# Kernel optimization log

Measured on AMD Instinct MI355X. Metric: run time of the kernel, lower is better.

The kernel has to match this reference:

```python
import jax, jax.numpy as jnp
import numpy as np

K = 5  # kernel_size


def _unfold(x, k):
    """Torch F.unfold equivalent: [B,C,H,W] -> [B,C,k*k,H,W].
    Patch index is row-major over the kxk window (dy*k+dx), matching
    F.unfold's channel-major / window-row-major layout after view(B,C,k*k,H,W)."""
    p = k // 2
    B, C, H, W = x.shape
    xp = jnp.pad(x, ((0, 0), (0, 0), (p, p), (p, p)))
    patches = [xp[:, :, dy:dy + H, dx:dx + W] for dy in range(k) for dx in range(k)]
    return jnp.stack(patches, axis=2)


def _conv2d(x, w, b, pad):
    y = jax.lax.conv_general_dilated(
        x, w, window_strides=(1, 1), padding=[(pad, pad), (pad, pad)],
        dimension_numbers=("NCHW", "OIHW", "NCHW"))
    return y + b[None, :, None, None]


def setup_inputs() -> dict:
    key = jax.random.key(0)
    k0, k1, k2 = jax.random.split(key, 3)
    B, H, W = 2, 1024, 1024
    flow = jax.random.normal(k0, (B, 2, H, W), jnp.float32)
    # kernel_gen params: Conv2d(3,32,3,pad=1) -> ReLU -> Conv2d(32,50,1)
    w1 = jax.random.normal(k1, (32, 3, 3, 3), jnp.float32) * 0.1
    b1 = jnp.zeros((32,), jnp.float32)
    w2 = jax.random.normal(k2, (K * K * 2, 32, 1, 1), jnp.float32) * 0.1
    b2 = jnp.zeros((K * K * 2,), jnp.float32)
    return {"flow": flow, "w1": w1, "b1": b1, "w2": w2, "b2": b2}


def reference(flow, w1, b1, w2, b2):
    B, _, H, W = flow.shape
    patches = _unfold(flow, K)                       # [B,2,25,H,W]
    # torch .var(dim=2) defaults to unbiased (ddof=1)
    var = jnp.var(patches, axis=2, ddof=1)           # [B,2,H,W]
    consistency = jnp.exp(-jnp.sqrt(jnp.sum(var * var, axis=1, keepdims=True)))  # [B,1,H,W]
    guidance = jnp.concatenate([flow, consistency], axis=1)  # [B,3,H,W]
    h = jax.nn.relu(_conv2d(guidance, w1, b1, pad=1))        # [B,32,H,W]
    kernels = _conv2d(h, w2, b2, pad=0).reshape(B, 2, K * K, H, W)
    refined = jnp.sum(kernels * patches, axis=2)             # [B,2,H,W]
    return refined
```

## Files before the change

### kernel.cpp

```cpp
#include <hip/hip_runtime.h>
#include <math.h>

#define KSZ 5
#define TSX 16
#define TSY 64
#define HALO 3
#define FWX 22
#define FH  70
#define SCH 66
#define PITCH 23
#define SF_C (FH*PITCH)
#define SC_BASE (2*SF_C)
#define SMF_TOT (SC_BASE + SCH*PITCH)

typedef __attribute__((ext_vector_type(8))) short short8_t;
typedef __attribute__((ext_vector_type(4))) float float4_t;
typedef __attribute__((ext_vector_type(2))) unsigned int uint2_t;

static __device__ __forceinline__ unsigned short f2bf(float f) {
    union { float f; unsigned int u; } v; v.f = f;
    return (unsigned short)((v.u + 0x7FFFu + ((v.u >> 16) & 1u)) >> 16);
}
static __device__ __forceinline__ unsigned int pk2t(float a, float b) {
    union { float f; unsigned int u; } ua, ub; ua.f = a; ub.f = b;
    return __builtin_amdgcn_perm(ub.u, ua.u, 0x07060302u);
}
static __device__ __forceinline__ float bflo(unsigned int u) {
    union { unsigned int u; float f; } v; v.u = u << 16; return v.f;
}
static __device__ __forceinline__ float bfhi(unsigned int u) {
    union { unsigned int u; float f; } v; v.u = u & 0xffff0000u; return v.f;
}

static __device__ __forceinline__ void slot_decode(int n, int& c, int& sel, int& idx, bool& valid) {
    int g4c = (n >> 2) & 3;
    c = g4c >> 1; sel = g4c & 1;
    idx = ((n >> 4) << 2) + (n & 3);
    valid = sel ? (idx < 10) : (idx < 15);
}

static __device__ __forceinline__ int kperm(int s) {
    int sg = s >> 3, sj = s & 7;
    if (sg < 3) return sg*9 + sj;
    if (sj == 1) return 8;
    if (sj == 2) return 17;
    if (sj == 4) return 26;
    return -1;
}

static __device__ __forceinline__ int kperm2(int s) {
    int g = s >> 3, j = s & 7;
    return (j < 4) ? (g*4 + j) : (16 + g*4 + (j - 4));
}

__global__ __launch_bounds__(256)
void pack_kernel(const float* __restrict__ w1, const float* __restrict__ b1,
                 const float* __restrict__ w2, const float* __restrict__ b2,
                 unsigned short* __restrict__ wp, float* __restrict__ bp)
{
    const int tid = threadIdx.x;
    for (int i = tid; i < 6*64*8; i += 256) {
        int f = i >> 9, l = (i >> 3) & 63, j = i & 7;
        int m = l & 15, s = ((l >> 4) << 3) + j;
        float v;
        if (f < 2) {
            int k = kperm(s);
            v = (k >= 0) ? w1[(f*16 + m)*27 + k] : 0.f;
        } else {
            int n = (f - 2)*16 + m;
            int c, sel, idx; bool valid;
            slot_decode(n, c, sel, idx, valid);
            v = valid ? w2[(c*25 + sel*15 + idx)*32 + kperm2(s)] : 0.f;
        }
        wp[i] = f2bf(v);
    }
    for (int i = tid; i < 6*64*4; i += 256) {
        int f = i >> 8, l = (i >> 2) & 63, r = i & 3, g4 = l >> 4;
        float v;
        if (f < 2) v = b1[f*16 + g4*4 + r];
        else {
            int n = (f - 2)*16 + g4*4 + r;
            int c, sel, idx; bool valid;
            slot_decode(n, c, sel, idx, valid);
            v = valid ? b2[c*25 + sel*15 + idx] : 0.f;
        }
        bp[i] = v;
    }
}

__global__ __launch_bounds__(256, 5)
void refine_kernel(const float* __restrict__ flow,
                   const unsigned short* __restrict__ wp,
                   const float* __restrict__ bp,
                   float* __restrict__ out, int H, int W)
{
    __shared__ float smf[SMF_TOT];
    __shared__ __align__(8) uint2_t rs[FH*18];

    const int tid = threadIdx.x;
    const int x0 = blockIdx.x * TSX;
    const int y0 = blockIdx.y * TSY;
    const int b  = blockIdx.z;

    const int lane = tid & 63;
    const int wave = tid >> 6;
    const int col  = lane & 15;
    const int g4   = lane >> 4;

    short8_t w1A[2], w2A[4];
    float4_t cb1[2], cb2[4];
    #pragma unroll
    for (int nt = 0; nt < 2; ++nt) {
        w1A[nt] = *(const short8_t*)&wp[(nt*64 + lane)*8];
        cb1[nt] = *(const float4_t*)&bp[(nt*64 + lane)*4];
    }
    #pragma unroll
    for (int nt = 0; nt < 4; ++nt) {
        w2A[nt] = *(const short8_t*)&wp[((2+nt)*64 + lane)*8];
        cb2[nt] = *(const float4_t*)&bp[((2+nt)*64 + lane)*4];
    }

    {
        const float* srcb = flow + (size_t)(b*2) * H * W;
        if (x0 >= 4 && x0 + TSX + 4 <= W && y0 >= HALO && y0 + TSY + HALO <= H) {
            const float* s = srcb + (size_t)(y0 - HALO) * W + (x0 - 4);
            for (int i = tid; i < 2*FH*12; i += 256) {
                int c = 0, r = i;
                if (r >= FH*12) { c = 1; r -= FH*12; }
                int ly = r / 12, lx2 = r - ly*12;
                float2 v = *(const float2*)(s + (size_t)c*H*W + (size_t)ly*W + 2*lx2);
                int dst = c*SF_C + ly*PITCH + 2*lx2 - 1;
                if (dst >= 0) smf[dst] = v.x;
                smf[dst + 1] = v.y;
            }
        } else {
            for (int i = tid; i < 2*FH*FWX; i += 256) {
                int c = 0, r = i;
                if (r >= FH*FWX) { c = 1; r -= FH*FWX; }
                int ly = r / FWX, lx = r - ly*FWX;
                int gy = y0 - HALO + ly, gx = x0 - HALO + lx;
                float v = 0.f;
                if (gy >= 0 && gy < H && gx >= 0 && gx < W)
                    v = srcb[(size_t)c*H*W + (size_t)gy*W + gx];
                smf[c*SF_C + ly*PITCH + lx] = v;
            }
        }
    }
    __syncthreads();

    for (int i = tid; i < FH*9; i += 256) {
        int y = i / 9, xp = (i - y*9) * 2;
        const float* r0 = &smf[y*PITCH + xp];
        const float* r1 = &smf[SF_C + y*PITCH + xp];
        float a0=r0[0], a1=r0[1], a2=r0[2], a3=r0[3], a4=r0[4], a5=r0[5];
        float c0=r1[0], c1=r1[1], c2=r1[2], c3=r1[3], c4=r1[4], c5=r1[5];
        float sA = ((a0+a1)+(a2+a3))+a4;
        float qA = fmaf(a4,a4, fmaf(a3,a3, fmaf(a2,a2, fmaf(a1,a1, a0*a0))));
        float sB = ((c0+c1)+(c2+c3))+c4;
        float qB = fmaf(c4,c4, fmaf(c3,c3, fmaf(c2,c2, fmaf(c1,c1, c0*c0))));
        float sA1 = sA + a5 - a0;
        float qA1 = fmaf(-a0, a0, fmaf(a5, a5, qA));
        float sB1 = sB + c5 - c0;
        float qB1 = fmaf(-c0, c0, fmaf(c5, c5, qB));
        rs[y*18 + xp]     = (uint2_t){pk2t(sA,  qA ), pk2t(sB,  qB )};
        rs[y*18 + xp + 1] = (uint2_t){pk2t(sA1, qA1), pk2t(sB1, qB1)};
    }
    __syncthreads();

    for (int i = tid; i < (SCH/2)*18; i += 256) {
        int u = i / 18, px = i - u*18;
        int py0 = u*2;
        int gx = x0 - 1 + px;
        int gy0 = y0 - 1 + py0;
        const uint2_t* rp = rs + py0*18 + px;
        float4_t f[6];
        #pragma unroll
        for (int k = 0; k < 6; ++k) {
            uint2_t uu = rp[k*18];
            f[k] = (float4_t){bflo(uu.x), bfhi(uu.x), bflo(uu.y), bfhi(uu.y)};
        }
        float4_t mid  = (f[1] + f[2]) + (f[3] + f[4]);
        float4_t acc0 = mid + f[0];
        float4_t acc1 = mid + f[5];
        float cons0 = 0.f, cons1 = 0.f;
        bool okx = (gx >= 0) && (gx < W);
        if (okx && gy0 >= 0 && gy0 < H) {
            float v0 = (acc0.y - acc0.x*acc0.x*(1.f/25.f)) * (1.f/24.f);
            float v1 = (acc0.w - acc0.z*acc0.z*(1.f/25.f)) * (1.f/24.f);
            cons0 = __expf(-sqrtf(v0*v0 + v1*v1));
        }
        if (okx && gy0+1 >= 0 && gy0+1 < H) {
            float v0 = (acc1.y - acc1.x*acc1.x*(1.f/25.f)) * (1.f/24.f);
            float v1 = (acc1.w - acc1.z*acc1.z*(1.f/25.f)) * (1.f/24.f);
            cons1 = __expf(-sqrtf(v0*v0 + v1*v1));
        }
        smf[SC_BASE + py0*PITCH + px]       = cons0;
        smf[SC_BASE + (py0+1)*PITCH + px]   = cons1;
    }
    __syncthreads();

    const int sel = g4 & 1, pc = g4 >> 1;
    const int ty0 = wave*16;

    int gb0, gb1, gb2, gb3;
    {
        int p0 = 0*SF_C + 2*PITCH + (col + 2);
        int p1 = 1*SF_C + 2*PITCH + (col + 2);
        int p2 = SC_BASE + col;
        if (g4 == 0)      { gb0 = gb1 = gb2 = gb3 = p0; }
        else if (g4 == 1) { gb0 = gb1 = gb2 = gb3 = p1; }
        else if (g4 == 2) { gb0 = gb1 = gb2 = gb3 = p2; }
        else { gb0 = p0 + 47; gb1 = p1 + 46; gb2 = p2 + 24; gb3 = p0; }
        gb0 += ty0*PITCH; gb1 += ty0*PITCH; gb2 += ty0*PITCH; gb3 += ty0*PITCH;
    }

    int pb = pc*SF_C + sel*(3*PITCH) + PITCH + 1 + col + ty0*PITCH;
    float pv[15];
    #pragma unroll
    for (int i = 0; i < 15; ++i) pv[i] = smf[pb + (i/5)*PITCH + (i%5)];

    #pragma unroll
    for (int mt = 0; mt < 16; ++mt) {
        float ga = smf[gb0 + 0],  gb_ = smf[gb0 + 1];
        float gc = smf[gb1 + 2],  gd  = smf[gb1 + 23];
        float ge = smf[gb2 + 24], gf  = smf[gb2 + 25];
        float gg = smf[gb3 + 46], gh  = smf[gb3 + 47];
        union { unsigned int u[4]; short8_t s; } gu;
        gu.u[0] = pk2t(ga, gb_); gu.u[1] = pk2t(gc, gd);
        gu.u[2] = pk2t(ge, gf);  gu.u[3] = pk2t(gg, gh);
        gb0 += PITCH; gb1 += PITCH; gb2 += PITCH; gb3 += PITCH;

        float4_t h0 = __builtin_amdgcn_mfma_f32_16x16x32_bf16(w1A[0], gu.s, cb1[0], 0, 0, 0);
        float4_t h1 = __builtin_amdgcn_mfma_f32_16x16x32_bf16(w1A[1], gu.s, cb1[1], 0, 0, 0);

        union { unsigned int u[4]; short8_t s; } hu;
        hu.u[0] = pk2t(fmaxf(h0[0],0.f), fmaxf(h0[1],0.f));
        hu.u[1] = pk2t(fmaxf(h0[2],0.f), fmaxf(h0[3],0.f));
        hu.u[2] = pk2t(fmaxf(h1[0],0.f), fmaxf(h1[1],0.f));
        hu.u[3] = pk2t(fmaxf(h1[2],0.f), fmaxf(h1[3],0.f));

        float4_t ka[4];
        #pragma unroll
        for (int nt = 0; nt < 4; ++nt)
            ka[nt] = __builtin_amdgcn_mfma_f32_16x16x32_bf16(w2A[nt], hu.s, cb2[nt], 0, 0, 0);

        float s = 0.f;
        #pragma unroll
        for (int i = 0; i < 15; ++i)
            s = fmaf(ka[i >> 2][i & 3], pv[i], s);

        if (mt < 15) {
            #pragma unroll
            for (int i = 0; i < 10; ++i) pv[i] = pv[i + 5];
            pb += PITCH;
            #pragma unroll
            for (int i = 10; i < 15; ++i) pv[i] = smf[pb + (i/5)*PITCH + (i%5)];
        }

        s += __shfl_xor(s, 16);

        if (sel == 0) {
            int y = y0 + ty0 + mt, x = x0 + col;
            out[((size_t)(b*2 + pc) * H + y) * W + x] = s;
        }
    }
}

extern "C" void kernel_launch(void* const* d_in, const int* in_sizes, int n_in,
                              void* d_out, int out_size, void* d_ws, size_t ws_size,
                              hipStream_t stream) {
    const float* flow = (const float*)d_in[0];
    const float* w1   = (const float*)d_in[1];
    const float* b1   = (const float*)d_in[2];
    const float* w2   = (const float*)d_in[3];
    const float* b2   = (const float*)d_in[4];
    float* out = (float*)d_out;

    unsigned short* wp = (unsigned short*)d_ws;
    float* bp = (float*)((char*)d_ws + 8192);

    const int H = 1024, W = 1024;
    const int B = in_sizes[0] / (2 * H * W);

    pack_kernel<<<1, 256, 0, stream>>>(w1, b1, w2, b2, wp, bp);
    dim3 grid(W / TSX, H / TSY, B);
    refine_kernel<<<grid, dim3(256), 0, stream>>>(flow, wp, bp, out, H, W);
}
```

Baseline: 109.8 us.

## Split row-sum stage into two halves to shrink LDS and raise occupancy

The horizontal row-sum buffer is cut from 70 rows to 38 by computing the consistency map in two passes, each filling the buffer and then reducing it vertically. The smaller LDS footprint lets the launch bound ask for 6 blocks per CU instead of 5, aiming at better latency hiding. ReLU is also applied as a vector max before packing. The price is two extra barriers and some recomputed halo rows, and the tighter register budget may cause spills.

```diff
diff --git a/kernel.cpp b/kernel.cpp
--- a/kernel.cpp
+++ b/kernel.cpp
@@ -12,6 +12,7 @@
 #define SF_C (FH*PITCH)
 #define SC_BASE (2*SF_C)
 #define SMF_TOT (SC_BASE + SCH*PITCH)
+#define RSROWS 38
 
 typedef __attribute__((ext_vector_type(8))) short short8_t;
 typedef __attribute__((ext_vector_type(4))) float float4_t;
@@ -30,6 +31,13 @@
 }
 static __device__ __forceinline__ float bfhi(unsigned int u) {
     union { unsigned int u; float f; } v; v.u = u & 0xffff0000u; return v.f;
+}
+static __device__ __forceinline__ float4_t relu4(float4_t x) {
+#if __has_builtin(__builtin_elementwise_max)
+    return __builtin_elementwise_max(x, (float4_t){0.f, 0.f, 0.f, 0.f});
+#else
+    return (float4_t){fmaxf(x[0],0.f), fmaxf(x[1],0.f), fmaxf(x[2],0.f), fmaxf(x[3],0.f)};
+#endif
 }
 
 static __device__ __forceinline__ void slot_decode(int n, int& c, int& sel, int& idx, bool& valid) {
@@ -88,14 +96,67 @@
     }
 }
 
-__global__ __launch_bounds__(256, 5)
+static __device__ __forceinline__ void hsum_row(const float* __restrict__ smf,
+                                                uint2_t* __restrict__ rs,
+                                                int y, int slot, int xp)
+{
+    const float* r0 = &smf[y*PITCH + xp];
+    const float* r1 = &smf[SF_C + y*PITCH + xp];
+    float a0=r0[0], a1=r0[1], a2=r0[2], a3=r0[3], a4=r0[4], a5=r0[5];
+    float c0=r1[0], c1=r1[1], c2=r1[2], c3=r1[3], c4=r1[4], c5=r1[5];
+    float sA = ((a0+a1)+(a2+a3))+a4;
+    float qA = fmaf(a4,a4, fmaf(a3,a3, fmaf(a2,a2, fmaf(a1,a1, a0*a0))));
+    float sB = ((c0+c1)+(c2+c3))+c4;
+    float qB = fmaf(c4,c4, fmaf(c3,c3, fmaf(c2,c2, fmaf(c1,c1, c0*c0))));
+    float sA1 = sA + a5 - a0;
+    float qA1 = fmaf(-a0, a0, fmaf(a5, a5, qA));
+    float sB1 = sB + c5 - c0;
+    float qB1 = fmaf(-c0, c0, fmaf(c5, c5, qB));
+    rs[slot*18 + xp]     = (uint2_t){pk2t(sA,  qA ), pk2t(sB,  qB )};
+    rs[slot*18 + xp + 1] = (uint2_t){pk2t(sA1, qA1), pk2t(sB1, qB1)};
+}
+
+static __device__ __forceinline__ void vsum_pair(float* __restrict__ smf,
+                                                 const uint2_t* __restrict__ rs,
+                                                 int slot0, int py0, int px,
+                                                 int x0, int y0, int H, int W)
+{
+    int gx = x0 - 1 + px;
+    int gy0 = y0 - 1 + py0;
+    const uint2_t* rp = rs + slot0*18 + px;
+    float4_t f[6];
+    #pragma unroll
+    for (int k = 0; k < 6; ++k) {
+        uint2_t uu = rp[k*18];
+        f[k] = (float4_t){bflo(uu.x), bfhi(uu.x), bflo(uu.y), bfhi(uu.y)};
+    }
+    float4_t mid  = (f[1] + f[2]) + (f[3] + f[4]);
+    float4_t acc0 = mid + f[0];
+    float4_t acc1 = mid + f[5];
+    float cons0 = 0.f, cons1 = 0.f;
+    bool okx = (gx >= 0) && (gx < W);
+    if (okx && gy0 >= 0 && gy0 < H) {
+        float v0 = (acc0.y - acc0.x*acc0.x*(1.f/25.f)) * (1.f/24.f);
+        float v1 = (acc0.w - acc0.z*acc0.z*(1.f/25.f)) * (1.f/24.f);
+        cons0 = __expf(-sqrtf(v0*v0 + v1*v1));
+    }
+    if (okx && gy0+1 >= 0 && gy0+1 < H) {
+        float v0 = (acc1.y - acc1.x*acc1.x*(1.f/25.f)) * (1.f/24.f);
+        float v1 = (acc1.w - acc1.z*acc1.z*(1.f/25.f)) * (1.f/24.f);
+        cons1 = __expf(-sqrtf(v0*v0 + v1*v1));
+    }
+    smf[SC_BASE + py0*PITCH + px]     = cons0;
+    smf[SC_BASE + (py0+1)*PITCH + px] = cons1;
+}
+
+__global__ __launch_bounds__(256, 6)
 void refine_kernel(const float* __restrict__ flow,
                    const unsigned short* __restrict__ wp,
                    const float* __restrict__ bp,
                    float* __restrict__ out, int H, int W)
 {
     __shared__ float smf[SMF_TOT];
-    __shared__ __align__(8) uint2_t rs[FH*18];
+    __shared__ __align__(8) uint2_t rs[RSROWS*18];
 
     const int tid = threadIdx.x;
     const int x0 = blockIdx.x * TSX;
@@ -148,54 +209,25 @@
     }
     __syncthreads();
 
-    for (int i = tid; i < FH*9; i += 256) {
+    for (int i = tid; i < RSROWS*9; i += 256) {
         int y = i / 9, xp = (i - y*9) * 2;
-        const float* r0 = &smf[y*PITCH + xp];
-        const float* r1 = &smf[SF_C + y*PITCH + xp];
-        float a0=r0[0], a1=r0[1], a2=r0[2], a3=r0[3], a4=r0[4], a5=r0[5];
-        float c0=r1[0], c1=r1[1], c2=r1[2], c3=r1[3], c4=r1[4], c5=r1[5];
-        float sA = ((a0+a1)+(a2+a3))+a4;
-        float qA = fmaf(a4,a4, fmaf(a3,a3, fmaf(a2,a2, fmaf(a1,a1, a0*a0))));
-        float sB = ((c0+c1)+(c2+c3))+c4;
-        float qB = fmaf(c4,c4, fmaf(c3,c3, fmaf(c2,c2, fmaf(c1,c1, c0*c0))));
-        float sA1 = sA + a5 - a0;
-        float qA1 = fmaf(-a0, a0, fmaf(a5, a5, qA));
-        float sB1 = sB + c5 - c0;
-        float qB1 = fmaf(-c0, c0, fmaf(c5, c5, qB));
-        rs[y*18 + xp]     = (uint2_t){pk2t(sA,  qA ), pk2t(sB,  qB )};
-        rs[y*18 + xp + 1] = (uint2_t){pk2t(sA1, qA1), pk2t(sB1, qB1)};
-    }
-    __syncthreads();
-
-    for (int i = tid; i < (SCH/2)*18; i += 256) {
+        hsum_row(smf, rs, y, y, xp);
+    }
+    __syncthreads();
+    for (int i = tid; i < 16*18; i += 256) {
         int u = i / 18, px = i - u*18;
-        int py0 = u*2;
-        int gx = x0 - 1 + px;
-        int gy0 = y0 - 1 + py0;
-        const uint2_t* rp = rs + py0*18 + px;
-        float4_t f[6];
-        #pragma unroll
-        for (int k = 0; k < 6; ++k) {
-            uint2_t uu = rp[k*18];
-            f[k] = (float4_t){bflo(uu.x), bfhi(uu.x), bflo(uu.y), bfhi(uu.y)};
-        }
-        float4_t mid  = (f[1] + f[2]) + (f[3] + f[4]);
-        float4_t acc0 = mid + f[0];
-        float4_t acc1 = mid + f[5];
-        float cons0 = 0.f, cons1 = 0.f;
-        bool okx = (gx >= 0) && (gx < W);
-        if (okx && gy0 >= 0 && gy0 < H) {
-            float v0 = (acc0.y - acc0.x*acc0.x*(1.f/25.f)) * (1.f/24.f);
-            float v1 = (acc0.w - acc0.z*acc0.z*(1.f/25.f)) * (1.f/24.f);
-            cons0 = __expf(-sqrtf(v0*v0 + v1*v1));
-        }
-        if (okx && gy0+1 >= 0 && gy0+1 < H) {
-            float v0 = (acc1.y - acc1.x*acc1.x*(1.f/25.f)) * (1.f/24.f);
-            float v1 = (acc1.w - acc1.z*acc1.z*(1.f/25.f)) * (1.f/24.f);
-            cons1 = __expf(-sqrtf(v0*v0 + v1*v1));
-        }
-        smf[SC_BASE + py0*PITCH + px]       = cons0;
-        smf[SC_BASE + (py0+1)*PITCH + px]   = cons1;
+        vsum_pair(smf, rs, u*2, u*2, px, x0, y0, H, W);
+    }
+    __syncthreads();
+
+    for (int i = tid; i < RSROWS*9; i += 256) {
+        int slot = i / 9, xp = (i - slot*9) * 2;
+        hsum_row(smf, rs, 32 + slot, slot, xp);
+    }
+    __syncthreads();
+    for (int i = tid; i < 17*18; i += 256) {
+        int u = i / 18, px = i - u*18;
+        vsum_pair(smf, rs, u*2, 32 + u*2, px, x0, y0, H, W);
     }
     __syncthreads();
 
@@ -232,12 +264,13 @@
 
         float4_t h0 = __builtin_amdgcn_mfma_f32_16x16x32_bf16(w1A[0], gu.s, cb1[0], 0, 0, 0);
         float4_t h1 = __builtin_amdgcn_mfma_f32_16x16x32_bf16(w1A[1], gu.s, cb1[1], 0, 0, 0);
+        h0 = relu4(h0); h1 = relu4(h1);
 
         union { unsigned int u[4]; short8_t s; } hu;
-        hu.u[0] = pk2t(fmaxf(h0[0],0.f), fmaxf(h0[1],0.f));
-        hu.u[1] = pk2t(fmaxf(h0[2],0.f), fmaxf(h0[3],0.f));
-        hu.u[2] = pk2t(fmaxf(h1[0],0.f), fmaxf(h1[1],0.f));
-        hu.u[3] = pk2t(fmaxf(h1[2],0.f), fmaxf(h1[3],0.f));
+        hu.u[0] = pk2t(h0[0], h0[1]);
+        hu.u[1] = pk2t(h0[2], h0[3]);
+        hu.u[2] = pk2t(h1[0], h1[1]);
+        hu.u[3] = pk2t(h1[2], h1[3]);
 
         float4_t ka[4];
         #pragma unroll
```

New measurement: 168.3 us. 53.2% more time.
